# Optimization experiments

Measured on AMD Instinct MI355X. Metric: run time of the kernel, lower is better.

The kernel has to match this reference:

```python
import jax, jax.numpy as jnp
import numpy as np

N = 100000
E = 1600000
F_IN = 128
HID = 64
N_CLS = 16


def gcn_conv(x, row, col, W, b, n_nodes):
    # x: [N, Fin]; row/col: [E+N] (self-loops already appended)
    h = x @ W  # [N, Fout]
    ones = jnp.ones(row.shape[0], dtype=x.dtype)
    deg = jax.ops.segment_sum(ones, col, num_segments=n_nodes)  # in-degree incl. self-loop
    dinv = jnp.where(deg > 0, jax.lax.rsqrt(deg), 0.0)
    norm = dinv[row] * dinv[col]  # [E+N]
    msg = h[row] * norm[:, None]  # gather + scale
    out = jax.ops.segment_sum(msg, col, num_segments=n_nodes)  # scatter-add
    return out + b


def setup_inputs() -> dict:
    key = jax.random.key(0)
    k1, k2, k3, k4, k5, k6 = jax.random.split(key, 6)
    x = jax.random.normal(k1, (N, F_IN), dtype=jnp.float32)
    edge_index = jax.random.randint(k2, (2, E), 0, N, dtype=jnp.int64)
    # Glorot-ish init for weights
    W1 = jax.random.normal(k3, (F_IN, HID), dtype=jnp.float32) / np.sqrt(F_IN)
    b1 = jnp.zeros((HID,), dtype=jnp.float32)
    W2 = jax.random.normal(k4, (HID, N_CLS), dtype=jnp.float32) / np.sqrt(HID)
    b2 = jnp.zeros((N_CLS,), dtype=jnp.float32)
    return {"x": x, "edge_index": edge_index, "W1": W1, "b1": b1, "W2": W2, "b2": b2}


def reference(x, edge_index, W1, b1, W2, b2):
    # Add self-loops (GCNConv default add_self_loops=True)
    loop = jnp.arange(N, dtype=edge_index.dtype)
    row = jnp.concatenate([edge_index[0], loop])
    col = jnp.concatenate([edge_index[1], loop])
    h = gcn_conv(x, row, col, W1, b1, N)
    h = jax.nn.relu(h)
    h = gcn_conv(h, row, col, W2, b2, N)
    return jax.nn.log_softmax(h, axis=1)
```

## Files before the change

### kernel.cpp

```cpp
#include <hip/hip_runtime.h>
#include <hip/hip_fp16.h>

#define F_IN 128
#define HID  64
#define NCLS 16
#define NPB  128
#define CAP  4096
#define CHUNK 4096
#define BINTHREADS 1024
#define GPAD 136

typedef _Float16 half_t;
typedef __attribute__((ext_vector_type(8))) _Float16 half8;
typedef __attribute__((ext_vector_type(4))) float float4v;


__global__ __launch_bounds__(BINTHREADS) void phaseA(
    const int* __restrict__ row, const int* __restrict__ col,
    int* __restrict__ cursor, int* __restrict__ ebuf, int E, int NB,
    const float* __restrict__ W1, half_t* __restrict__ W1t, int nblkE)
{
    if ((int)blockIdx.x >= nblkE) {
        for (int i = threadIdx.x; i < F_IN * HID; i += BINTHREADS) {
            int k = i >> 6, n = i & 63;
            W1t[n * F_IN + k] = (half_t)W1[i];
        }
        return;
    }
    __shared__ int hist[1024], base[1024], off[1024];
    for (int i = threadIdx.x; i < NB; i += BINTHREADS) hist[i] = 0;
    int e0 = blockIdx.x * CHUNK + threadIdx.x * 4;
    int nv = min(max(E - e0, 0), 4);
    int4 c4 = make_int4(0, 0, 0, 0), r4 = make_int4(0, 0, 0, 0);
    if (nv == 4) {
        c4 = *(const int4*)&col[e0];
        r4 = *(const int4*)&row[e0];
    } else {
        if (nv > 0) { c4.x = col[e0 + 0]; r4.x = row[e0 + 0]; }
        if (nv > 1) { c4.y = col[e0 + 1]; r4.y = row[e0 + 1]; }
        if (nv > 2) { c4.z = col[e0 + 2]; r4.z = row[e0 + 2]; }
    }
    __syncthreads();
    if (nv > 0) atomicAdd(&hist[c4.x >> 7], 1);
    if (nv > 1) atomicAdd(&hist[c4.y >> 7], 1);
    if (nv > 2) atomicAdd(&hist[c4.z >> 7], 1);
    if (nv > 3) atomicAdd(&hist[c4.w >> 7], 1);
    __syncthreads();
    for (int i = threadIdx.x; i < NB; i += BINTHREADS) {
        int h = hist[i];
        base[i] = h ? (i * CAP + atomicAdd(&cursor[i], h)) : 0;
        off[i] = 0;
    }
    __syncthreads();
    if (nv > 0) { int b = c4.x >> 7; int p = base[b] + atomicAdd(&off[b], 1);
                  if (p < (b + 1) * CAP) ebuf[p] = (r4.x << 7) | (c4.x & (NPB - 1)); }
    if (nv > 1) { int b = c4.y >> 7; int p = base[b] + atomicAdd(&off[b], 1);
                  if (p < (b + 1) * CAP) ebuf[p] = (r4.y << 7) | (c4.y & (NPB - 1)); }
    if (nv > 2) { int b = c4.z >> 7; int p = base[b] + atomicAdd(&off[b], 1);
                  if (p < (b + 1) * CAP) ebuf[p] = (r4.z << 7) | (c4.z & (NPB - 1)); }
    if (nv > 3) { int b = c4.w >> 7; int p = base[b] + atomicAdd(&off[b], 1);
                  if (p < (b + 1) * CAP) ebuf[p] = (r4.w << 7) | (c4.w & (NPB - 1)); }
}


__global__ __launch_bounds__(1024, 8) void phaseB_gemm1(
    const int* __restrict__ ebuf, const int* __restrict__ cursor,
    const float* __restrict__ x, const half_t* __restrict__ W1t,
    int2* __restrict__ rsc, int* __restrict__ csr_row,
    __half* __restrict__ hs1, int N)
{
    __shared__ int hist[NPB], cur[NPB];
    __shared__ int wtot, cnt_s;
    __shared__ float dv[NPB];
    __shared__ __align__(16) half_t As[NPB * GPAD];
    int t = threadIdx.x;
    int b = blockIdx.x;
    int node0 = b << 7;
    int ebase = b * CAP;
    if (t == 0) cnt_s = min(cursor[b], CAP);
    if (t < NPB) hist[t] = 0;

    float4 xv[4];
    size_t total = (size_t)N * F_IN;
    #pragma unroll
    for (int i = 0; i < 4; ++i) {
        int f = i * 1024 + t;
        int nl = f >> 5, k4 = f & 31;
        size_t g = (size_t)(node0 + nl) * F_IN + k4 * 4;
        xv[i] = make_float4(0.f, 0.f, 0.f, 0.f);
        if (g < total) xv[i] = *(const float4*)&x[g];
    }
    __syncthreads();
    int cnt = cnt_s;

    int p0 = (t < cnt)        ? ebuf[ebase + t]        : -1;
    int p1 = (t + 1024 < cnt) ? ebuf[ebase + t + 1024] : -1;
    if (p0 >= 0) atomicAdd(&hist[p0 & (NPB - 1)], 1);
    if (p1 >= 0) atomicAdd(&hist[p1 & (NPB - 1)], 1);
    if (cnt > 2048)
        for (int e = 2048 + t; e < cnt; e += 1024)
            atomicAdd(&hist[ebuf[ebase + e] & (NPB - 1)], 1);

    #pragma unroll
    for (int i = 0; i < 4; ++i) {
        int f = i * 1024 + t;
        int nl = f >> 5, k4 = f & 31;
        half_t* dst = &As[nl * GPAD + k4 * 4];
        dst[0] = (half_t)xv[i].x; dst[1] = (half_t)xv[i].y;
        dst[2] = (half_t)xv[i].z; dst[3] = (half_t)xv[i].w;
    }
    __syncthreads();

    int h = 0, incl = 0;
    if (t < NPB) {
        h = hist[t];
        incl = h;
        #pragma unroll
        for (int off = 1; off < 64; off <<= 1) {
            int u = __shfl_up(incl, off, 64);
            if ((t & 63) >= off) incl += u;
        }
        if (t == 63) wtot = incl;
    }
    __syncthreads();
    if (t < NPB) {
        if (t >= 64) incl += wtot;
        int start = ebase + incl - h;
        cur[t] = start;
        dv[t] = rsqrtf((float)h + 1.0f);
        int n = node0 + t;
        if (n < N) rsc[n] = make_int2(start, h);
    }
    __syncthreads();

    if (p0 >= 0) { int pos = atomicAdd(&cur[p0 & (NPB - 1)], 1); csr_row[pos] = p0 >> 7; }
    if (p1 >= 0) { int pos = atomicAdd(&cur[p1 & (NPB - 1)], 1); csr_row[pos] = p1 >> 7; }
    if (cnt > 2048)
        for (int e = 2048 + t; e < cnt; e += 1024) {
            int p = ebuf[ebase + e];
            int pos = atomicAdd(&cur[p & (NPB - 1)], 1);
            csr_row[pos] = p >> 7;
        }

    int wv = t >> 6, lane = t & 63;
    int l15 = lane & 15, quad = lane >> 4;
    int mrow0 = (wv & 7) * 16;
    int fcol0 = (wv >> 3) * 16;
    float4v acc0 = {0.f, 0.f, 0.f, 0.f};
    float4v acc1 = {0.f, 0.f, 0.f, 0.f};
    #pragma unroll
    for (int kb = 0; kb < 4; ++kb) {
        half8 a  = *(const half8*)&As[(mrow0 + l15) * GPAD + kb * 32 + quad * 8];
        half8 b0 = *(const half8*)&W1t[(size_t)(fcol0 + l15) * F_IN + kb * 32 + quad * 8];
        half8 b1 = *(const half8*)&W1t[(size_t)(fcol0 + 32 + l15) * F_IN + kb * 32 + quad * 8];
        acc0 = __builtin_amdgcn_mfma_f32_16x16x32_f16(a, b0, acc0, 0, 0, 0);
        acc1 = __builtin_amdgcn_mfma_f32_16x16x32_f16(a, b1, acc1, 0, 0, 0);
    }
    #pragma unroll
    for (int r = 0; r < 4; ++r) {
        int m = mrow0 + quad * 4 + r;
        int n = node0 + m;
        if (n < N) {
            float d = dv[m];
            hs1[(size_t)n * HID + fcol0 + l15]      = __float2half(acc0[r] * d);
            hs1[(size_t)n * HID + fcol0 + 32 + l15] = __float2half(acc1[r] * d);
        }
    }
}


__global__ __launch_bounds__(256) void agg_l1(
    const __half* __restrict__ hs1, const int2* __restrict__ rsc,
    const int* __restrict__ csr, const float* __restrict__ b1,
    const float* __restrict__ W2, __half* __restrict__ h2s, int N)
{
    __shared__ float W2l[HID * NCLS];
    __shared__ float o1[32][65];
    for (int i = threadIdx.x; i < HID * NCLS; i += 256) W2l[i] = W2[i];
    __syncthreads();
    int w = threadIdx.x >> 6, lane = threadIdx.x & 63;
    int g = lane >> 3, gl = lane & 7;
    int rowi = w * 8 + g;
    int c = blockIdx.x * 32 + rowi;
    bool active = (c < N);
    int cc = active ? c : 0;
    int2 rc = rsc[cc];
    int e0 = rc.x, e1 = rc.x + rc.y;
    int e1m1 = e1 - 1;
    float dc = rsqrtf((float)rc.y + 1.0f);
    const half8* H = (const half8*)hs1;
    half8 sv = H[(size_t)cc * 8 + gl];
    float sum[8];
    #pragma unroll
    for (int k = 0; k < 8; ++k) sum[k] = (float)sv[k];
    for (int i = e0; i < e1; i += 8) {
        int id[8];
        #pragma unroll
        for (int s = 0; s < 8; ++s) id[s] = csr[min(i + s, e1m1)];
        half8 a[8];
        #pragma unroll
        for (int s = 0; s < 8; ++s) a[s] = H[(size_t)id[s] * 8 + gl];
        #pragma unroll
        for (int s = 0; s < 8; ++s) {
            float fm = (i + s < e1) ? 1.f : 0.f;
            #pragma unroll
            for (int k = 0; k < 8; ++k) sum[k] = fmaf(fm, (float)a[s][k], sum[k]);
        }
    }
    float4 bb0 = *(const float4*)&b1[gl * 8];
    float4 bb1 = *(const float4*)&b1[gl * 8 + 4];
    o1[rowi][gl * 8 + 0] = fmaxf(fmaf(dc, sum[0], bb0.x), 0.f);
    o1[rowi][gl * 8 + 1] = fmaxf(fmaf(dc, sum[1], bb0.y), 0.f);
    o1[rowi][gl * 8 + 2] = fmaxf(fmaf(dc, sum[2], bb0.z), 0.f);
    o1[rowi][gl * 8 + 3] = fmaxf(fmaf(dc, sum[3], bb0.w), 0.f);
    o1[rowi][gl * 8 + 4] = fmaxf(fmaf(dc, sum[4], bb1.x), 0.f);
    o1[rowi][gl * 8 + 5] = fmaxf(fmaf(dc, sum[5], bb1.y), 0.f);
    o1[rowi][gl * 8 + 6] = fmaxf(fmaf(dc, sum[6], bb1.z), 0.f);
    o1[rowi][gl * 8 + 7] = fmaxf(fmaf(dc, sum[7], bb1.w), 0.f);
    int j0 = gl * 2, j1 = gl * 2 + 1;
    float s0 = 0.f, s1 = 0.f;
    const float* orow = o1[rowi];
    #pragma unroll 8
    for (int k = 0; k < HID; ++k) {
        float ov = orow[k];
        s0 = fmaf(ov, W2l[k * NCLS + j0], s0);
        s1 = fmaf(ov, W2l[k * NCLS + j1], s1);
    }
    if (active) {
        __half2 hv;
        hv.x = __float2half(dc * s0);
        hv.y = __float2half(dc * s1);
        ((__half2*)h2s)[(size_t)c * 8 + gl] = hv;
    }
}


__global__ __launch_bounds__(256) void agg2_final(
    const __half* __restrict__ h2s, const int2* __restrict__ rsc,
    const int* __restrict__ csr, const float* __restrict__ b2,
    float* __restrict__ out, int N)
{
    int lane = threadIdx.x & 63;
    int g = lane >> 3, gl = lane & 7;
    int c = blockIdx.x * 32 + (threadIdx.x >> 6) * 8 + g;
    bool active = (c < N);
    int cc = active ? c : 0;
    int2 rc = rsc[cc];
    int e0 = rc.x, e1 = rc.x + rc.y;
    int e1m1 = e1 - 1;
    float dcv = rsqrtf((float)rc.y + 1.0f);
    const __half2* H = (const __half2*)h2s;
    float2 sum = __half22float2(H[(size_t)cc * 8 + gl]);
    for (int i = e0; i < e1; i += 8) {
        int id[8];
        #pragma unroll
        for (int s = 0; s < 8; ++s) id[s] = csr[min(i + s, e1m1)];
        __half2 a[8];
        #pragma unroll
        for (int s = 0; s < 8; ++s) a[s] = H[(size_t)id[s] * 8 + gl];
        #pragma unroll
        for (int s = 0; s < 8; ++s) {
            float fm = (i + s < e1) ? 1.f : 0.f;
            float2 f2 = __half22float2(a[s]);
            sum.x = fmaf(fm, f2.x, sum.x);
            sum.y = fmaf(fm, f2.y, sum.y);
        }
    }
    float2 bb = ((const float2*)b2)[gl];
    float2 v;
    v.x = fmaf(dcv, sum.x, bb.x);
    v.y = fmaf(dcv, sum.y, bb.y);
    float mx = fmaxf(v.x, v.y);
    mx = fmaxf(mx, __shfl_xor(mx, 1, 64));
    mx = fmaxf(mx, __shfl_xor(mx, 2, 64));
    mx = fmaxf(mx, __shfl_xor(mx, 4, 64));
    float s = __expf(v.x - mx) + __expf(v.y - mx);
    s += __shfl_xor(s, 1, 64);
    s += __shfl_xor(s, 2, 64);
    s += __shfl_xor(s, 4, 64);
    float lse = mx + __logf(s);
    if (active) ((float2*)out)[(size_t)c * 8 + gl] = make_float2(v.x - lse, v.y - lse);
}


extern "C" void kernel_launch(void* const* d_in, const int* in_sizes, int n_in,
                              void* d_out, int out_size, void* d_ws, size_t ws_size,
                              hipStream_t stream) {
    const float* x  = (const float*)d_in[0];
    const int*   ei = (const int*)d_in[1];
    const float* W1 = (const float*)d_in[2];
    const float* b1 = (const float*)d_in[3];
    const float* W2 = (const float*)d_in[4];
    const float* b2 = (const float*)d_in[5];
    float* out = (float*)d_out;

    const int N = in_sizes[0] / F_IN;
    const int E = in_sizes[1] / 2;
    const int* row = ei;
    const int* col = ei + E;

    const int NB = (N + NPB - 1) / NPB;
    size_t Np  = ((size_t)N + 15) & ~(size_t)15;
    size_t NBp = ((size_t)NB + 15) & ~(size_t)15;
    size_t Rg  = (size_t)NB * CAP;

    char* p = (char*)d_ws;
    __half* hs1     = (__half*)p;  p += Np * HID * 2;
    __half* h2s     = (__half*)p;  p += Np * NCLS * 2;
    half_t* W1t     = (half_t*)p;  p += (size_t)F_IN * HID * 2;
    int2*   rsc     = (int2*)p;    p += Np * 8;
    int*    csr_row = (int*)p;     p += Rg * 4;
    int*    ebuf    = (int*)p;     p += Rg * 4;
    int*    cursor  = (int*)p;     p += NBp * 4;

    int nblkE = (E + CHUNK - 1) / CHUNK;

    hipMemsetAsync(cursor, 0, NBp * sizeof(int), stream);
    phaseA<<<nblkE + 1, BINTHREADS, 0, stream>>>(row, col, cursor, ebuf, E, NB, W1, W1t, nblkE);
    phaseB_gemm1<<<NB, 1024, 0, stream>>>(ebuf, cursor, x, W1t, rsc, csr_row, hs1, N);
    agg_l1<<<(N + 31) / 32, 256, 0, stream>>>(hs1, rsc, csr_row, b1, W2, h2s, N);
    agg2_final<<<(N + 31) / 32, 256, 0, stream>>>(h2s, rsc, csr_row, b2, out, N);
}
```

Before: 190.8 us.

## Shrink phaseB to 256 threads and feed MFMA directly from global x

Reduces the CSR-build plus GEMM1 kernel from 1024 to 256 threads per block. Each thread now preloads 8 edge entries, and each wave computes 32 rows by 64 columns with MFMA. The A operand is read straight from global x and converted to fp16 in registers, which removes the LDS staging buffer and one barrier. This lowers LDS use and allows more blocks per CU, at the cost of more registers per thread and fewer threads doing the atomic histogram and scatter work. The preload reads ebuf slots past cnt unconditionally; they stay inside the block's CAP region and are masked before use.

```diff
diff --git a/kernel.cpp b/kernel.cpp
--- a/kernel.cpp
+++ b/kernel.cpp
@@ -8,7 +8,6 @@
 #define CAP  4096
 #define CHUNK 4096
 #define BINTHREADS 1024
-#define GPAD 136
 
 typedef _Float16 half_t;
 typedef __attribute__((ext_vector_type(8))) _Float16 half8;
@@ -63,52 +62,32 @@
 }
 
 
-__global__ __launch_bounds__(1024, 8) void phaseB_gemm1(
+__global__ __launch_bounds__(256) void phaseB_gemm1(
     const int* __restrict__ ebuf, const int* __restrict__ cursor,
     const float* __restrict__ x, const half_t* __restrict__ W1t,
     int2* __restrict__ rsc, int* __restrict__ csr_row,
     __half* __restrict__ hs1, int N)
 {
     __shared__ int hist[NPB], cur[NPB];
-    __shared__ int wtot, cnt_s;
+    __shared__ int wtot;
     __shared__ float dv[NPB];
-    __shared__ __align__(16) half_t As[NPB * GPAD];
     int t = threadIdx.x;
     int b = blockIdx.x;
     int node0 = b << 7;
     int ebase = b * CAP;
-    if (t == 0) cnt_s = min(cursor[b], CAP);
+
+    int p[8];
+    #pragma unroll
+    for (int k = 0; k < 8; ++k) p[k] = ebuf[ebase + t + 256 * k];
+    int cnt = min(cursor[b], CAP);
     if (t < NPB) hist[t] = 0;
-
-    float4 xv[4];
-    size_t total = (size_t)N * F_IN;
-    #pragma unroll
-    for (int i = 0; i < 4; ++i) {
-        int f = i * 1024 + t;
-        int nl = f >> 5, k4 = f & 31;
-        size_t g = (size_t)(node0 + nl) * F_IN + k4 * 4;
-        xv[i] = make_float4(0.f, 0.f, 0.f, 0.f);
-        if (g < total) xv[i] = *(const float4*)&x[g];
-    }
-    __syncthreads();
-    int cnt = cnt_s;
-
-    int p0 = (t < cnt)        ? ebuf[ebase + t]        : -1;
-    int p1 = (t + 1024 < cnt) ? ebuf[ebase + t + 1024] : -1;
-    if (p0 >= 0) atomicAdd(&hist[p0 & (NPB - 1)], 1);
-    if (p1 >= 0) atomicAdd(&hist[p1 & (NPB - 1)], 1);
+    __syncthreads();
+    #pragma unroll
+    for (int k = 0; k < 8; ++k)
+        if (t + 256 * k < cnt) atomicAdd(&hist[p[k] & (NPB - 1)], 1);
     if (cnt > 2048)
-        for (int e = 2048 + t; e < cnt; e += 1024)
+        for (int e = 2048 + t; e < cnt; e += 256)
             atomicAdd(&hist[ebuf[ebase + e] & (NPB - 1)], 1);
-
-    #pragma unroll
-    for (int i = 0; i < 4; ++i) {
-        int f = i * 1024 + t;
-        int nl = f >> 5, k4 = f & 31;
-        half_t* dst = &As[nl * GPAD + k4 * 4];
-        dst[0] = (half_t)xv[i].x; dst[1] = (half_t)xv[i].y;
-        dst[2] = (half_t)xv[i].z; dst[3] = (half_t)xv[i].w;
-    }
     __syncthreads();
 
     int h = 0, incl = 0;
@@ -133,39 +112,60 @@
     }
     __syncthreads();
 
-    if (p0 >= 0) { int pos = atomicAdd(&cur[p0 & (NPB - 1)], 1); csr_row[pos] = p0 >> 7; }
-    if (p1 >= 0) { int pos = atomicAdd(&cur[p1 & (NPB - 1)], 1); csr_row[pos] = p1 >> 7; }
+    #pragma unroll
+    for (int k = 0; k < 8; ++k)
+        if (t + 256 * k < cnt) {
+            int pos = atomicAdd(&cur[p[k] & (NPB - 1)], 1);
+            csr_row[pos] = p[k] >> 7;
+        }
     if (cnt > 2048)
-        for (int e = 2048 + t; e < cnt; e += 1024) {
-            int p = ebuf[ebase + e];
-            int pos = atomicAdd(&cur[p & (NPB - 1)], 1);
-            csr_row[pos] = p >> 7;
+        for (int e = 2048 + t; e < cnt; e += 256) {
+            int pp = ebuf[ebase + e];
+            int pos = atomicAdd(&cur[pp & (NPB - 1)], 1);
+            csr_row[pos] = pp >> 7;
         }
 
     int wv = t >> 6, lane = t & 63;
     int l15 = lane & 15, quad = lane >> 4;
-    int mrow0 = (wv & 7) * 16;
-    int fcol0 = (wv >> 3) * 16;
-    float4v acc0 = {0.f, 0.f, 0.f, 0.f};
-    float4v acc1 = {0.f, 0.f, 0.f, 0.f};
+    int mbase = wv * 32;
+    int r0 = min(node0 + mbase + l15, N - 1);
+    int r1 = min(node0 + mbase + 16 + l15, N - 1);
+    const float* x0 = x + (size_t)r0 * F_IN;
+    const float* x1 = x + (size_t)r1 * F_IN;
+    float4v acc[2][4];
+    #pragma unroll
+    for (int mt = 0; mt < 2; ++mt)
+        #pragma unroll
+        for (int j = 0; j < 4; ++j) acc[mt][j] = (float4v){0.f, 0.f, 0.f, 0.f};
     #pragma unroll
     for (int kb = 0; kb < 4; ++kb) {
-        half8 a  = *(const half8*)&As[(mrow0 + l15) * GPAD + kb * 32 + quad * 8];
-        half8 b0 = *(const half8*)&W1t[(size_t)(fcol0 + l15) * F_IN + kb * 32 + quad * 8];
-        half8 b1 = *(const half8*)&W1t[(size_t)(fcol0 + 32 + l15) * F_IN + kb * 32 + quad * 8];
-        acc0 = __builtin_amdgcn_mfma_f32_16x16x32_f16(a, b0, acc0, 0, 0, 0);
-        acc1 = __builtin_amdgcn_mfma_f32_16x16x32_f16(a, b1, acc1, 0, 0, 0);
-    }
-    #pragma unroll
-    for (int r = 0; r < 4; ++r) {
-        int m = mrow0 + quad * 4 + r;
-        int n = node0 + m;
-        if (n < N) {
-            float d = dv[m];
-            hs1[(size_t)n * HID + fcol0 + l15]      = __float2half(acc0[r] * d);
-            hs1[(size_t)n * HID + fcol0 + 32 + l15] = __float2half(acc1[r] * d);
-        }
-    }
+        int off = kb * 32 + quad * 8;
+        float4 fa = *(const float4*)&x0[off];
+        float4 fb = *(const float4*)&x0[off + 4];
+        float4 ga = *(const float4*)&x1[off];
+        float4 gb = *(const float4*)&x1[off + 4];
+        half8 a0 = {(half_t)fa.x, (half_t)fa.y, (half_t)fa.z, (half_t)fa.w,
+                    (half_t)fb.x, (half_t)fb.y, (half_t)fb.z, (half_t)fb.w};
+        half8 a1 = {(half_t)ga.x, (half_t)ga.y, (half_t)ga.z, (half_t)ga.w,
+                    (half_t)gb.x, (half_t)gb.y, (half_t)gb.z, (half_t)gb.w};
+        #pragma unroll
+        for (int j = 0; j < 4; ++j) {
+            half8 bv = *(const half8*)&W1t[(size_t)(j * 16 + l15) * F_IN + off];
+            acc[0][j] = __builtin_amdgcn_mfma_f32_16x16x32_f16(a0, bv, acc[0][j], 0, 0, 0);
+            acc[1][j] = __builtin_amdgcn_mfma_f32_16x16x32_f16(a1, bv, acc[1][j], 0, 0, 0);
+        }
+    }
+    #pragma unroll
+    for (int mt = 0; mt < 2; ++mt)
+        #pragma unroll
+        for (int j = 0; j < 4; ++j)
+            #pragma unroll
+            for (int r = 0; r < 4; ++r) {
+                int m = mbase + mt * 16 + quad * 4 + r;
+                int n = node0 + m;
+                if (n < N) hs1[(size_t)n * HID + j * 16 + l15] =
+                    __float2half(acc[mt][j][r] * dv[m]);
+            }
 }
 
 
@@ -317,7 +317,7 @@
 
     hipMemsetAsync(cursor, 0, NBp * sizeof(int), stream);
     phaseA<<<nblkE + 1, BINTHREADS, 0, stream>>>(row, col, cursor, ebuf, E, NB, W1, W1t, nblkE);
-    phaseB_gemm1<<<NB, 1024, 0, stream>>>(ebuf, cursor, x, W1t, rsc, csr_row, hs1, N);
+    phaseB_gemm1<<<NB, 256, 0, stream>>>(ebuf, cursor, x, W1t, rsc, csr_row, hs1, N);
     agg_l1<<<(N + 31) / 32, 256, 0, stream>>>(hs1, rsc, csr_row, b1, W2, h2s, N);
     agg2_final<<<(N + 31) / 32, 256, 0, stream>>>(h2s, rsc, csr_row, b2, out, N);
 }
```

Measured after the change: 192.0 us. About the same (+0.6%).
